# Kernel optimization log

Measured on AMD Instinct MI355X. Metric: run time of the kernel, lower is better.

Reference implementation:

```python
import jax, jax.numpy as jnp
import numpy as np

N_NODES = 100000
N_EDGES = 1600000
IN_CH, HID_CH, OUT_CH = 128, 128, 64


def glorot(key, fan_in, fan_out):
    lim = np.sqrt(6.0 / (fan_in + fan_out)).astype(np.float32)
    return jax.random.uniform(key, (fan_in, fan_out), jnp.float32, -lim, lim)


def gcn_conv(x, src, dst, W, b):
    """PyG GCNConv: add self-loops, symmetric deg^-1/2 normalization,
    linear transform, scatter-add aggregation at targets, plus bias."""
    n = x.shape[0]
    xw = x @ W  # [N, F_out]
    loop = jnp.arange(n)
    s = jnp.concatenate([src, loop])  # sources (message origin)
    d = jnp.concatenate([dst, loop])  # targets (aggregation site)
    deg = jax.ops.segment_sum(jnp.ones_like(d, dtype=xw.dtype), d, num_segments=n)
    dinv = jnp.where(deg > 0, jax.lax.rsqrt(deg), 0.0)
    norm = dinv[s] * dinv[d]  # [E+N]
    out = jax.ops.segment_sum(norm[:, None] * xw[s], d, num_segments=n)
    return out + b


def setup_inputs() -> dict:
    key = jax.random.key(0)
    ks = jax.random.split(key, 8)
    x = jax.random.normal(ks[0], (N_NODES, IN_CH), jnp.float32)
    edge_index = jax.random.randint(ks[1], (2, N_EDGES), 0, N_NODES, jnp.int64)
    return {
        "x": x,
        "edge_index": edge_index,
        "W1": glorot(ks[2], IN_CH, HID_CH),
        "b1": jnp.zeros((HID_CH,), jnp.float32),
        "W2": glorot(ks[3], HID_CH, HID_CH),
        "b2": jnp.zeros((HID_CH,), jnp.float32),
        "W3": glorot(ks[4], HID_CH, OUT_CH),
        "b3": jnp.zeros((OUT_CH,), jnp.float32),
    }


def reference(x, edge_index, W1, b1, W2, b2, W3, b3):
    src, dst = edge_index[0], edge_index[1]
    # eval mode: dropout is identity
    h = jax.nn.relu(gcn_conv(x, src, dst, W1, b1))
    h = jax.nn.relu(gcn_conv(h, src, dst, W2, b2))
    h = gcn_conv(h, src, dst, W3, b3)
    return jax.nn.log_softmax(h, axis=1)
```

## Files before the change

kernel.cpp:

```cpp
#include <hip/hip_runtime.h>
#include <math.h>


#define NN 100000
#define NE 1600000
#define NBUK 391
#define BCAP 4608

typedef float floatx4 __attribute__((ext_vector_type(4)));
typedef short short8 __attribute__((ext_vector_type(8)));

__device__ __forceinline__ unsigned short f2bf(float f) {
    unsigned u = __float_as_uint(f);
    unsigned r = (u + 0x7fffu + ((u >> 16) & 1u)) >> 16;
    return (unsigned short)r;
}
__device__ __forceinline__ float bflo(unsigned u) { return __uint_as_float(u << 16); }
__device__ __forceinline__ float bfhi(unsigned u) { return __uint_as_float(u & 0xffff0000u); }

__global__ __launch_bounds__(256) void k_wprep(const float* __restrict__ W, unsigned short* __restrict__ Wtg,
                                               int K, int NC) {
    int idx = blockIdx.x * 256 + threadIdx.x;
    if (idx >= NC * K) return;
    int n = idx / K, k = idx - n * K;
    Wtg[idx] = f2bf(W[k * NC + n]);
}

__global__ __launch_bounds__(256) void k_bucket(const int4* __restrict__ src4, const int4* __restrict__ dst4,
                                                int* __restrict__ bcur, int* __restrict__ bbuf, int E) {
    __shared__ int hist[NBUK];
    __shared__ int base[NBUK];
    int t = threadIdx.x;
    for (int b = t; b < NBUK; b += 256) hist[b] = 0;
    __syncthreads();
    int E4 = E >> 2;
    int q0 = blockIdx.x * 1024;
    #pragma unroll
    for (int j = 0; j < 4; j++) {
        int q = q0 + j * 256 + t;
        if (q < E4) {
            int4 d = dst4[q];
            atomicAdd(&hist[d.x >> 8], 1);
            atomicAdd(&hist[d.y >> 8], 1);
            atomicAdd(&hist[d.z >> 8], 1);
            atomicAdd(&hist[d.w >> 8], 1);
        }
    }
    __syncthreads();
    for (int b = t; b < NBUK; b += 256) {
        int c = hist[b];
        base[b] = c ? atomicAdd(&bcur[b], c) : 0;
        hist[b] = 0;
    }
    __syncthreads();
    #pragma unroll
    for (int j = 0; j < 4; j++) {
        int q = q0 + j * 256 + t;
        if (q < E4) {
            int4 s = src4[q];
            int4 d = dst4[q];
            int sv[4] = {s.x, s.y, s.z, s.w};
            int dv[4] = {d.x, d.y, d.z, d.w};
            #pragma unroll
            for (int u = 0; u < 4; u++) {
                int b = dv[u] >> 8;
                int r = atomicAdd(&hist[b], 1);
                int pos = base[b] + r;
                if (pos < BCAP) bbuf[b * BCAP + pos] = (sv[u] << 8) | (dv[u] & 255);
            }
        }
    }
}

__global__ void k_scanbuckets(const int* __restrict__ bcur, int* __restrict__ bbase, int nb,
                              int* __restrict__ row_ptr, int n, int E) {
    int lane = threadIdx.x;
    int carry = 0;
    for (int base = 0; base < nb; base += 64) {
        int idx = base + lane;
        int v = (idx < nb) ? min(bcur[idx], BCAP) : 0;
        int orig = v;
        #pragma unroll
        for (int o = 1; o < 64; o <<= 1) {
            int u = __shfl_up(v, o);
            if (lane >= o) v += u;
        }
        if (idx < nb) bbase[idx] = carry + v - orig;
        carry += __shfl(v, 63);
    }
    if (lane == 0) row_ptr[n] = E;
}

__global__ __launch_bounds__(256) void k_build(const int* __restrict__ bcur, const int* __restrict__ bbase,
                                               const int* __restrict__ bbuf,
                                               int* __restrict__ row_ptr, int* __restrict__ csr, int N) {
    __shared__ int sh[256];
    __shared__ int cur[256];
    __shared__ int loc[BCAP];
    int b = blockIdx.x, t = threadIdx.x;
    int cnt = min(bcur[b], BCAP);
    int gbase = bbase[b];
    const int* bp = bbuf + b * BCAP;
    sh[t] = 0;
    __syncthreads();
    for (int i = t; i < cnt; i += 256) atomicAdd(&sh[bp[i] & 255], 1);
    __syncthreads();
    int v = sh[t];
    for (int o = 1; o < 256; o <<= 1) {
        int u = (t >= o) ? sh[t - o] : 0;
        __syncthreads();
        sh[t] += u;
        __syncthreads();
    }
    int excl = sh[t] - v;
    int node = b * 256 + t;
    if (node < N) row_ptr[node] = gbase + excl;
    cur[t] = excl;
    __syncthreads();
    for (int i = t; i < cnt; i += 256) {
        int p = bp[i];
        int r = atomicAdd(&cur[p & 255], 1);
        loc[r] = p >> 8;
    }
    __syncthreads();
    for (int i = t; i < cnt; i += 256) csr[gbase + i] = loc[i];
}

__global__ __launch_bounds__(256) void k_dinv(const int* __restrict__ row_ptr, float* __restrict__ dinv, int n) {
    int i = blockIdx.x * 256 + threadIdx.x;
    if (i < n) {
        int d = row_ptr[i + 1] - row_ptr[i];
        dinv[i] = rsqrtf((float)d + 1.0f);
    }
}


template <int NC, bool CVT>
__global__ __launch_bounds__(256) void k_mfma(const void* __restrict__ Av, const unsigned short* __restrict__ Wtg,
                                              const float* __restrict__ dinv, unsigned short* __restrict__ Y, int M) {
    constexpr int K = 128;
    constexpr int NT = NC / 16;
    constexpr int NU = NC / 32;
    __shared__ unsigned short Wt[NC][136];
    __shared__ unsigned short Ost[4][16][NC + 8];
    int t = threadIdx.x;
    constexpr int NV = NC * K / 8;
    for (int idx = t; idx < NV; idx += 256) {
        int nrow = idx >> 4;
        int chunk = idx & 15;
        *(uint4*)&Wt[nrow][chunk * 8] = *(const uint4*)(Wtg + nrow * K + chunk * 8);
    }
    __syncthreads();
    int lane = t & 63, wid = t >> 6;
    int col = lane & 15, quad = lane >> 4;
    int nstrips = M / 16;
    int stride = gridDim.x * 4;
    int s = blockIdx.x * 4 + wid;
    if (s >= nstrips) return;

    auto loadA = [&](int strip, short8 af[4]) {
        int row0 = strip * 16;
        if (CVT) {
            const float* Af = (const float*)Av + (size_t)(row0 + col) * K + quad * 8;
            #pragma unroll
            for (int ks = 0; ks < 4; ks++) {
                float4 f0 = *(const float4*)(Af + ks * 32);
                float4 f1 = *(const float4*)(Af + ks * 32 + 4);
                short8 v;
                v[0] = (short)f2bf(f0.x); v[1] = (short)f2bf(f0.y); v[2] = (short)f2bf(f0.z); v[3] = (short)f2bf(f0.w);
                v[4] = (short)f2bf(f1.x); v[5] = (short)f2bf(f1.y); v[6] = (short)f2bf(f1.z); v[7] = (short)f2bf(f1.w);
                af[ks] = v;
            }
        } else {
            const unsigned short* Ab = (const unsigned short*)Av + (size_t)(row0 + col) * K + quad * 8;
            #pragma unroll
            for (int ks = 0; ks < 4; ks++) af[ks] = *(const short8*)(Ab + ks * 32);
        }
    };

    short8 cur[4];
    loadA(s, cur);
    while (true) {
        int snext = s + stride;
        bool has = (snext < nstrips);
        short8 nxt[4];
        if (has) loadA(snext, nxt);

        floatx4 acc[NT];
        #pragma unroll
        for (int i = 0; i < NT; i++) acc[i] = (floatx4){0.f, 0.f, 0.f, 0.f};
        #pragma unroll
        for (int ks = 0; ks < 4; ks++) {
            #pragma unroll
            for (int nt = 0; nt < NT; nt++) {
                short8 bfrag = *(const short8*)&Wt[nt * 16 + col][ks * 32 + quad * 8];
                acc[nt] = __builtin_amdgcn_mfma_f32_16x16x32_bf16(cur[ks], bfrag, acc[nt], 0, 0, 0);
            }
        }
        int row0 = s * 16;
        #pragma unroll
        for (int r = 0; r < 4; r++) {
            int row = row0 + quad * 4 + r;
            float dv = dinv[row];
            #pragma unroll
            for (int nt = 0; nt < NT; nt++) {
                Ost[wid][quad * 4 + r][nt * 16 + col] = f2bf(acc[nt][r] * dv);
            }
        }
        #pragma unroll
        for (int i = 0; i < NU; i++) {
            int idx = i * 64 + lane;
            int rr = idx >> 4, cc = idx & 15;
            int rr2 = (NC == 128) ? (idx >> 4) : (idx >> 3);
            int cc2 = (NC == 128) ? (idx & 15) : (idx & 7);
            (void)rr; (void)cc;
            ((uint4*)&Y[(size_t)(row0 + rr2) * NC])[cc2] = *(uint4*)&Ost[wid][rr2][cc2 * 8];
        }
        if (!has) break;
        s = snext;
        #pragma unroll
        for (int ks = 0; ks < 4; ks++) cur[ks] = nxt[ks];
    }
}


__device__ __forceinline__ void acc8(float* a, uint4 v) {
    a[0] += bflo(v.x); a[1] += bfhi(v.x);
    a[2] += bflo(v.y); a[3] += bfhi(v.y);
    a[4] += bflo(v.z); a[5] += bfhi(v.z);
    a[6] += bflo(v.w); a[7] += bfhi(v.w);
}

__global__ __launch_bounds__(256) void k_gather_relu_bf(const uint4* __restrict__ y, const int* __restrict__ csr,
                                                        const int* __restrict__ row_ptr, const float* __restrict__ dinv,
                                                        const float* __restrict__ bias, uint4* __restrict__ h, int n) {
    int node = blockIdx.x * 16 + (threadIdx.x >> 4);
    int c = threadIdx.x & 15;
    if (node >= n) return;
    int s0 = row_ptr[node], s1 = row_ptr[node + 1];
    float a[8] = {};
    acc8(a, y[(size_t)node * 16 + c]);
    int p = s0;
    for (; p + 4 <= s1; p += 4) {
        int i0 = csr[p], i1 = csr[p + 1], i2 = csr[p + 2], i3 = csr[p + 3];
        uint4 v0 = y[(size_t)i0 * 16 + c];
        uint4 v1 = y[(size_t)i1 * 16 + c];
        uint4 v2 = y[(size_t)i2 * 16 + c];
        uint4 v3 = y[(size_t)i3 * 16 + c];
        acc8(a, v0); acc8(a, v1); acc8(a, v2); acc8(a, v3);
    }
    for (; p < s1; p++) acc8(a, y[(size_t)csr[p] * 16 + c]);
    float s = dinv[node];
    float4 b0 = ((const float4*)bias)[c * 2];
    float4 b1 = ((const float4*)bias)[c * 2 + 1];
    float r0 = fmaxf(s * a[0] + b0.x, 0.f), r1 = fmaxf(s * a[1] + b0.y, 0.f);
    float r2 = fmaxf(s * a[2] + b0.z, 0.f), r3 = fmaxf(s * a[3] + b0.w, 0.f);
    float r4 = fmaxf(s * a[4] + b1.x, 0.f), r5 = fmaxf(s * a[5] + b1.y, 0.f);
    float r6 = fmaxf(s * a[6] + b1.z, 0.f), r7 = fmaxf(s * a[7] + b1.w, 0.f);
    uint4 o;
    o.x = ((unsigned)f2bf(r1) << 16) | f2bf(r0);
    o.y = ((unsigned)f2bf(r3) << 16) | f2bf(r2);
    o.z = ((unsigned)f2bf(r5) << 16) | f2bf(r4);
    o.w = ((unsigned)f2bf(r7) << 16) | f2bf(r6);
    h[(size_t)node * 16 + c] = o;
}

__global__ __launch_bounds__(256) void k_gather_lsm_bf(const uint4* __restrict__ y, const int* __restrict__ csr,
                                                       const int* __restrict__ row_ptr, const float* __restrict__ dinv,
                                                       const float* __restrict__ bias, float4* __restrict__ out4, int n) {
    int node = blockIdx.x * 32 + (threadIdx.x >> 3);
    int c = threadIdx.x & 7;
    if (node >= n) return;
    int s0 = row_ptr[node], s1 = row_ptr[node + 1];
    float a[8] = {};
    acc8(a, y[(size_t)node * 8 + c]);
    int p = s0;
    for (; p + 4 <= s1; p += 4) {
        int i0 = csr[p], i1 = csr[p + 1], i2 = csr[p + 2], i3 = csr[p + 3];
        uint4 v0 = y[(size_t)i0 * 8 + c];
        uint4 v1 = y[(size_t)i1 * 8 + c];
        uint4 v2 = y[(size_t)i2 * 8 + c];
        uint4 v3 = y[(size_t)i3 * 8 + c];
        acc8(a, v0); acc8(a, v1); acc8(a, v2); acc8(a, v3);
    }
    for (; p < s1; p++) acc8(a, y[(size_t)csr[p] * 8 + c]);
    float s = dinv[node];
    float4 b0 = ((const float4*)bias)[c * 2];
    float4 b1 = ((const float4*)bias)[c * 2 + 1];
    float v[8];
    v[0] = s * a[0] + b0.x; v[1] = s * a[1] + b0.y; v[2] = s * a[2] + b0.z; v[3] = s * a[3] + b0.w;
    v[4] = s * a[4] + b1.x; v[5] = s * a[5] + b1.y; v[6] = s * a[6] + b1.z; v[7] = s * a[7] + b1.w;
    float m = v[0];
    #pragma unroll
    for (int i = 1; i < 8; i++) m = fmaxf(m, v[i]);
    #pragma unroll
    for (int o = 4; o > 0; o >>= 1) m = fmaxf(m, __shfl_xor(m, o));
    float sum = 0.f;
    #pragma unroll
    for (int i = 0; i < 8; i++) sum += expf(v[i] - m);
    #pragma unroll
    for (int o = 4; o > 0; o >>= 1) sum += __shfl_xor(sum, o);
    float lse = m + logf(sum);
    out4[(size_t)node * 16 + c * 2]     = make_float4(v[0] - lse, v[1] - lse, v[2] - lse, v[3] - lse);
    out4[(size_t)node * 16 + c * 2 + 1] = make_float4(v[4] - lse, v[5] - lse, v[6] - lse, v[7] - lse);
}


extern "C" void kernel_launch(void* const* d_in, const int* in_sizes, int n_in,
                              void* d_out, int out_size, void* d_ws, size_t ws_size,
                              hipStream_t stream) {
    const float* x  = (const float*)d_in[0];
    const int*   ei = (const int*)d_in[1];
    const float* W1 = (const float*)d_in[2];
    const float* b1 = (const float*)d_in[3];
    const float* W2 = (const float*)d_in[4];
    const float* b2 = (const float*)d_in[5];
    const float* W3 = (const float*)d_in[6];
    const float* b3 = (const float*)d_in[7];
    float* out = (float*)d_out;

    const int N = NN, E = NE;
    const int nb = (N + 255) / 256;

    char* ws = (char*)d_ws;
    size_t off = 0;
    auto alloc = [&](size_t bytes) -> void* {
        void* p = ws + off;
        off += bytes;
        off = (off + 255) & ~(size_t)255;
        return p;
    };
    int*            row_ptr = (int*)alloc((size_t)(N + 1) * 4);
    float*          dinvv   = (float*)alloc((size_t)N * 4);
    int*            bcur    = (int*)alloc(512 * 4);
    int*            bbase   = (int*)alloc(512 * 4);
    int*            bbuf    = (int*)alloc((size_t)NBUK * BCAP * 4);
    int*            csr     = (int*)alloc((size_t)E * 4);
    unsigned short* wt1     = (unsigned short*)alloc(128 * 128 * 2);
    unsigned short* wt2     = (unsigned short*)alloc(128 * 128 * 2);
    unsigned short* wt3     = (unsigned short*)alloc(64 * 128 * 2);
    unsigned short* yb      = (unsigned short*)alloc((size_t)N * 128 * 2);
    unsigned short* hb      = (unsigned short*)alloc((size_t)N * 128 * 2);
    (void)ws_size; (void)in_sizes; (void)n_in; (void)out_size;

    const int* srcp = ei;
    const int* dstp = ei + E;

    hipMemsetAsync(bcur, 0, 512 * 4, stream);
    k_wprep<<<64, 256, 0, stream>>>(W1, wt1, 128, 128);
    k_wprep<<<64, 256, 0, stream>>>(W2, wt2, 128, 128);
    k_wprep<<<32, 256, 0, stream>>>(W3, wt3, 128, 64);
    k_bucket<<<(E + 4095) / 4096, 256, 0, stream>>>((const int4*)srcp, (const int4*)dstp, bcur, bbuf, E);
    k_scanbuckets<<<1, 64, 0, stream>>>(bcur, bbase, NBUK, row_ptr, N, E);
    k_build<<<NBUK, 256, 0, stream>>>(bcur, bbase, bbuf, row_ptr, csr, N);
    k_dinv<<<nb, 256, 0, stream>>>(row_ptr, dinvv, N);

    k_mfma<128, true><<<512, 256, 0, stream>>>(x, wt1, dinvv, yb, N);
    k_gather_relu_bf<<<N / 16, 256, 0, stream>>>((const uint4*)yb, csr, row_ptr, dinvv, b1, (uint4*)hb, N);
    k_mfma<128, false><<<512, 256, 0, stream>>>(hb, wt2, dinvv, yb, N);
    k_gather_relu_bf<<<N / 16, 256, 0, stream>>>((const uint4*)yb, csr, row_ptr, dinvv, b2, (uint4*)hb, N);
    k_mfma<64, false><<<512, 256, 0, stream>>>(hb, wt3, dinvv, yb, N);
    k_gather_lsm_bf<<<N / 32, 256, 0, stream>>>((const uint4*)yb, csr, row_ptr, dinvv, b3, (float4*)out, N);
}
```

Measured before the change: 336.1 us.

## Fuse gather+ReLU with next layer's MFMA transform into one persistent kernel

Measured after the change: 343.4 us. 1.02x slower.

```diff
diff --git a/kernel.cpp b/kernel.cpp
--- a/kernel.cpp
+++ b/kernel.cpp
@@ -135,19 +135,14 @@
 }
 
 
-template <int NC, bool CVT>
-__global__ __launch_bounds__(256) void k_mfma(const void* __restrict__ Av, const unsigned short* __restrict__ Wtg,
-                                              const float* __restrict__ dinv, unsigned short* __restrict__ Y, int M) {
-    constexpr int K = 128;
-    constexpr int NT = NC / 16;
-    constexpr int NU = NC / 32;
+__global__ __launch_bounds__(256) void k_mfma1(const float* __restrict__ Av, const unsigned short* __restrict__ Wtg,
+                                               const float* __restrict__ dinv, unsigned short* __restrict__ Y, int M) {
+    constexpr int K = 128, NC = 128, NT = 8, NU = 4;
     __shared__ unsigned short Wt[NC][136];
     __shared__ unsigned short Ost[4][16][NC + 8];
     int t = threadIdx.x;
-    constexpr int NV = NC * K / 8;
-    for (int idx = t; idx < NV; idx += 256) {
-        int nrow = idx >> 4;
-        int chunk = idx & 15;
+    for (int idx = t; idx < NC * 16; idx += 256) {
+        int nrow = idx >> 4, chunk = idx & 15;
         *(uint4*)&Wt[nrow][chunk * 8] = *(const uint4*)(Wtg + nrow * K + chunk * 8);
     }
     __syncthreads();
@@ -159,22 +154,15 @@
     if (s >= nstrips) return;
 
     auto loadA = [&](int strip, short8 af[4]) {
-        int row0 = strip * 16;
-        if (CVT) {
-            const float* Af = (const float*)Av + (size_t)(row0 + col) * K + quad * 8;
-            #pragma unroll
-            for (int ks = 0; ks < 4; ks++) {
-                float4 f0 = *(const float4*)(Af + ks * 32);
-                float4 f1 = *(const float4*)(Af + ks * 32 + 4);
-                short8 v;
-                v[0] = (short)f2bf(f0.x); v[1] = (short)f2bf(f0.y); v[2] = (short)f2bf(f0.z); v[3] = (short)f2bf(f0.w);
-                v[4] = (short)f2bf(f1.x); v[5] = (short)f2bf(f1.y); v[6] = (short)f2bf(f1.z); v[7] = (short)f2bf(f1.w);
-                af[ks] = v;
-            }
-        } else {
-            const unsigned short* Ab = (const unsigned short*)Av + (size_t)(row0 + col) * K + quad * 8;
-            #pragma unroll
-            for (int ks = 0; ks < 4; ks++) af[ks] = *(const short8*)(Ab + ks * 32);
+        const float* Af = Av + (size_t)(strip * 16 + col) * K + quad * 8;
+        #pragma unroll
+        for (int ks = 0; ks < 4; ks++) {
+            float4 f0 = *(const float4*)(Af + ks * 32);
+            float4 f1 = *(const float4*)(Af + ks * 32 + 4);
+            short8 v;
+            v[0] = (short)f2bf(f0.x); v[1] = (short)f2bf(f0.y); v[2] = (short)f2bf(f0.z); v[3] = (short)f2bf(f0.w);
+            v[4] = (short)f2bf(f1.x); v[5] = (short)f2bf(f1.y); v[6] = (short)f2bf(f1.z); v[7] = (short)f2bf(f1.w);
+            af[ks] = v;
         }
     };
 
@@ -200,21 +188,16 @@
         int row0 = s * 16;
         #pragma unroll
         for (int r = 0; r < 4; r++) {
-            int row = row0 + quad * 4 + r;
-            float dv = dinv[row];
+            float dv = dinv[row0 + quad * 4 + r];
             #pragma unroll
-            for (int nt = 0; nt < NT; nt++) {
+            for (int nt = 0; nt < NT; nt++)
                 Ost[wid][quad * 4 + r][nt * 16 + col] = f2bf(acc[nt][r] * dv);
-            }
         }
         #pragma unroll
         for (int i = 0; i < NU; i++) {
             int idx = i * 64 + lane;
             int rr = idx >> 4, cc = idx & 15;
-            int rr2 = (NC == 128) ? (idx >> 4) : (idx >> 3);
-            int cc2 = (NC == 128) ? (idx & 15) : (idx & 7);
-            (void)rr; (void)cc;
-            ((uint4*)&Y[(size_t)(row0 + rr2) * NC])[cc2] = *(uint4*)&Ost[wid][rr2][cc2 * 8];
+            ((uint4*)&Y[(size_t)(row0 + rr) * NC])[cc] = *(uint4*)&Ost[wid][rr][cc * 8];
         }
         if (!has) break;
         s = snext;
@@ -231,38 +214,114 @@
     a[6] += bflo(v.w); a[7] += bfhi(v.w);
 }
 
-__global__ __launch_bounds__(256) void k_gather_relu_bf(const uint4* __restrict__ y, const int* __restrict__ csr,
-                                                        const int* __restrict__ row_ptr, const float* __restrict__ dinv,
-                                                        const float* __restrict__ bias, uint4* __restrict__ h, int n) {
-    int node = blockIdx.x * 16 + (threadIdx.x >> 4);
-    int c = threadIdx.x & 15;
-    if (node >= n) return;
-    int s0 = row_ptr[node], s1 = row_ptr[node + 1];
-    float a[8] = {};
-    acc8(a, y[(size_t)node * 16 + c]);
-    int p = s0;
-    for (; p + 4 <= s1; p += 4) {
-        int i0 = csr[p], i1 = csr[p + 1], i2 = csr[p + 2], i3 = csr[p + 3];
-        uint4 v0 = y[(size_t)i0 * 16 + c];
-        uint4 v1 = y[(size_t)i1 * 16 + c];
-        uint4 v2 = y[(size_t)i2 * 16 + c];
-        uint4 v3 = y[(size_t)i3 * 16 + c];
-        acc8(a, v0); acc8(a, v1); acc8(a, v2); acc8(a, v3);
-    }
-    for (; p < s1; p++) acc8(a, y[(size_t)csr[p] * 16 + c]);
-    float s = dinv[node];
+template <int NCOUT>
+__global__ __launch_bounds__(256) void k_gather_mfma(const uint4* __restrict__ y, const int* __restrict__ csr,
+                                                     const int* __restrict__ row_ptr, const float* __restrict__ dinv,
+                                                     const float* __restrict__ bias,
+                                                     const unsigned short* __restrict__ Wtg,
+                                                     unsigned short* __restrict__ Yout, int M) {
+    constexpr int K = 128;
+    constexpr int CW = NCOUT / 4;
+    constexpr int NTW = CW / 16;
+    __shared__ unsigned short Wt[NCOUT][136];
+    __shared__ unsigned short Hs[16][136];
+    __shared__ unsigned short Ys[4][16][CW + 8];
+
+    int t = threadIdx.x;
+    for (int idx = t; idx < NCOUT * 16; idx += 256) {
+        int nrow = idx >> 4, chunk = idx & 15;
+        *(uint4*)&Wt[nrow][chunk * 8] = *(const uint4*)(Wtg + nrow * K + chunk * 8);
+    }
+    __syncthreads();
+
+    int lane = t & 63, wid = t >> 6;
+    int col = lane & 15, quad = lane >> 4;
+    int m = t >> 4;
+    int c = t & 15;
     float4 b0 = ((const float4*)bias)[c * 2];
     float4 b1 = ((const float4*)bias)[c * 2 + 1];
-    float r0 = fmaxf(s * a[0] + b0.x, 0.f), r1 = fmaxf(s * a[1] + b0.y, 0.f);
-    float r2 = fmaxf(s * a[2] + b0.z, 0.f), r3 = fmaxf(s * a[3] + b0.w, 0.f);
-    float r4 = fmaxf(s * a[4] + b1.x, 0.f), r5 = fmaxf(s * a[5] + b1.y, 0.f);
-    float r6 = fmaxf(s * a[6] + b1.z, 0.f), r7 = fmaxf(s * a[7] + b1.w, 0.f);
-    uint4 o;
-    o.x = ((unsigned)f2bf(r1) << 16) | f2bf(r0);
-    o.y = ((unsigned)f2bf(r3) << 16) | f2bf(r2);
-    o.z = ((unsigned)f2bf(r5) << 16) | f2bf(r4);
-    o.w = ((unsigned)f2bf(r7) << 16) | f2bf(r6);
-    h[(size_t)node * 16 + c] = o;
+
+    int nstrips = M / 16;
+    for (int s = blockIdx.x; s < nstrips; s += gridDim.x) {
+        int node = s * 16 + m;
+        int s0 = row_ptr[node], s1 = row_ptr[node + 1];
+        float a[8] = {};
+        acc8(a, y[(size_t)node * 16 + c]);
+        int p = s0;
+        int i0, i1, i2, i3, i4, i5, i6, i7;
+        if (p + 8 <= s1) {
+            i0 = csr[p]; i1 = csr[p+1]; i2 = csr[p+2]; i3 = csr[p+3];
+            i4 = csr[p+4]; i5 = csr[p+5]; i6 = csr[p+6]; i7 = csr[p+7];
+            while (true) {
+                uint4 v0 = y[(size_t)i0 * 16 + c], v1 = y[(size_t)i1 * 16 + c];
+                uint4 v2 = y[(size_t)i2 * 16 + c], v3 = y[(size_t)i3 * 16 + c];
+                uint4 v4 = y[(size_t)i4 * 16 + c], v5 = y[(size_t)i5 * 16 + c];
+                uint4 v6 = y[(size_t)i6 * 16 + c], v7 = y[(size_t)i7 * 16 + c];
+                p += 8;
+                bool nxt = (p + 8 <= s1);
+                if (nxt) {
+                    i0 = csr[p]; i1 = csr[p+1]; i2 = csr[p+2]; i3 = csr[p+3];
+                    i4 = csr[p+4]; i5 = csr[p+5]; i6 = csr[p+6]; i7 = csr[p+7];
+                }
+                acc8(a, v0); acc8(a, v1); acc8(a, v2); acc8(a, v3);
+                acc8(a, v4); acc8(a, v5); acc8(a, v6); acc8(a, v7);
+                if (!nxt) break;
+            }
+        }
+        if (p + 4 <= s1) {
+            int j0 = csr[p], j1 = csr[p+1], j2 = csr[p+2], j3 = csr[p+3];
+            uint4 v0 = y[(size_t)j0 * 16 + c], v1 = y[(size_t)j1 * 16 + c];
+            uint4 v2 = y[(size_t)j2 * 16 + c], v3 = y[(size_t)j3 * 16 + c];
+            acc8(a, v0); acc8(a, v1); acc8(a, v2); acc8(a, v3);
+            p += 4;
+        }
+        for (; p < s1; p++) acc8(a, y[(size_t)csr[p] * 16 + c]);
+        float sc = dinv[node];
+        float r0 = fmaxf(sc * a[0] + b0.x, 0.f), r1 = fmaxf(sc * a[1] + b0.y, 0.f);
+        float r2 = fmaxf(sc * a[2] + b0.z, 0.f), r3 = fmaxf(sc * a[3] + b0.w, 0.f);
+        float r4 = fmaxf(sc * a[4] + b1.x, 0.f), r5 = fmaxf(sc * a[5] + b1.y, 0.f);
+        float r6 = fmaxf(sc * a[6] + b1.z, 0.f), r7 = fmaxf(sc * a[7] + b1.w, 0.f);
+        uint4 o;
+        o.x = ((unsigned)f2bf(r1) << 16) | f2bf(r0);
+        o.y = ((unsigned)f2bf(r3) << 16) | f2bf(r2);
+        o.z = ((unsigned)f2bf(r5) << 16) | f2bf(r4);
+        o.w = ((unsigned)f2bf(r7) << 16) | f2bf(r6);
+        *(uint4*)&Hs[m][c * 8] = o;
+        __syncthreads();
+
+        floatx4 acc[NTW];
+        #pragma unroll
+        for (int j = 0; j < NTW; j++) acc[j] = (floatx4){0.f, 0.f, 0.f, 0.f};
+        #pragma unroll
+        for (int ks = 0; ks < 4; ks++) {
+            short8 af = *(const short8*)&Hs[col][ks * 32 + quad * 8];
+            #pragma unroll
+            for (int j = 0; j < NTW; j++) {
+                short8 bf = *(const short8*)&Wt[wid * CW + j * 16 + col][ks * 32 + quad * 8];
+                acc[j] = __builtin_amdgcn_mfma_f32_16x16x32_bf16(af, bf, acc[j], 0, 0, 0);
+            }
+        }
+        #pragma unroll
+        for (int r = 0; r < 4; r++) {
+            int rr = quad * 4 + r;
+            float dv = dinv[s * 16 + rr];
+            #pragma unroll
+            for (int j = 0; j < NTW; j++)
+                Ys[wid][rr][j * 16 + col] = f2bf(acc[j][r] * dv);
+        }
+        if (NCOUT == 128) {
+            int rr = lane >> 2, cc = lane & 3;
+            uint4 v = *(uint4*)&Ys[wid][rr][cc * 8];
+            *(uint4*)&Yout[(size_t)(s * 16 + rr) * NCOUT + wid * CW + cc * 8] = v;
+        } else {
+            if (lane < 32) {
+                int rr = lane >> 1, cc = lane & 1;
+                uint4 v = *(uint4*)&Ys[wid][rr][cc * 8];
+                *(uint4*)&Yout[(size_t)(s * 16 + rr) * NCOUT + wid * CW + cc * 8] = v;
+            }
+        }
+        __syncthreads();
+    }
 }
 
 __global__ __launch_bounds__(256) void k_gather_lsm_bf(const uint4* __restrict__ y, const int* __restrict__ csr,
@@ -340,7 +399,8 @@
     unsigned short* wt2     = (unsigned short*)alloc(128 * 128 * 2);
     unsigned short* wt3     = (unsigned short*)alloc(64 * 128 * 2);
     unsigned short* yb      = (unsigned short*)alloc((size_t)N * 128 * 2);
-    unsigned short* hb      = (unsigned short*)alloc((size_t)N * 128 * 2);
+    unsigned short* y2      = (unsigned short*)alloc((size_t)N * 128 * 2);
+    unsigned short* y3      = (unsigned short*)alloc((size_t)N * 64 * 2);
     (void)ws_size; (void)in_sizes; (void)n_in; (void)out_size;
 
     const int* srcp = ei;
@@ -355,10 +415,8 @@
     k_build<<<NBUK, 256, 0, stream>>>(bcur, bbase, bbuf, row_ptr, csr, N);
     k_dinv<<<nb, 256, 0, stream>>>(row_ptr, dinvv, N);
 
-    k_mfma<128, true><<<512, 256, 0, stream>>>(x, wt1, dinvv, yb, N);
-    k_gather_relu_bf<<<N / 16, 256, 0, stream>>>((const uint4*)yb, csr, row_ptr, dinvv, b1, (uint4*)hb, N);
-    k_mfma<128, false><<<512, 256, 0, stream>>>(hb, wt2, dinvv, yb, N);
-    k_gather_relu_bf<<<N / 16, 256, 0, stream>>>((const uint4*)yb, csr, row_ptr, dinvv, b2, (uint4*)hb, N);
-    k_mfma<64, false><<<512, 256, 0, stream>>>(hb, wt3, dinvv, yb, N);
-    k_gather_lsm_bf<<<N / 32, 256, 0, stream>>>((const uint4*)yb, csr, row_ptr, dinvv, b3, (float4*)out, N);
-}
+    k_mfma1<<<512, 256, 0, stream>>>(x, wt1, dinvv, yb, N);
+    k_gather_mfma<128><<<1024, 256, 0, stream>>>((const uint4*)yb, csr, row_ptr, dinvv, b1, wt2, y2, N);
+    k_gather_mfma<64><<<1024, 256, 0, stream>>>((const uint4*)y2, csr, row_ptr, dinvv, b2, wt3, y3, N);
+    k_gather_lsm_bf<<<N / 32, 256, 0, stream>>>((const uint4*)y3, csr, row_ptr, dinvv, b3, (float4*)out, N);
+}
```
